# Kernel optimization log

Measured on AMD Instinct MI355X. Metric: run time of the kernel, lower is better.

Reference implementation:

```python
import jax, jax.numpy as jnp
import numpy as np
import math

HIDDEN = 768
HEADS = 12
HEAD_DIM = HIDDEN // HEADS
BLOCK = 256
TOPK = 3
BATCH = 2
SEQ = 2048


def setup_inputs() -> dict:
    key = jax.random.key(0)
    ks = jax.random.split(key, 5)
    s = 1.0 / math.sqrt(HIDDEN)
    return {
        "hidden_states": jax.random.normal(ks[0], (BATCH, SEQ, HIDDEN), jnp.float32),
        "Wq": jax.random.normal(ks[1], (HIDDEN, HIDDEN), jnp.float32) * s,
        "Wk": jax.random.normal(ks[2], (HIDDEN, HIDDEN), jnp.float32) * s,
        "Wv": jax.random.normal(ks[3], (HIDDEN, HIDDEN), jnp.float32) * s,
        "Wo": jax.random.normal(ks[4], (HIDDEN, HIDDEN), jnp.float32) * s,
    }


def _rope(x, sin, cos):
    # x: [B, H, S, D]; rotate-half RoPE
    d2 = x.shape[-1] // 2
    x1, x2 = x[..., :d2], x[..., d2:]
    return x * cos + jnp.concatenate([-x2, x1], axis=-1) * sin


def reference(hidden_states, Wq, Wk, Wv, Wo):
    B, S, Hd = hidden_states.shape
    H, D, bs, K = HEADS, HEAD_DIM, BLOCK, TOPK
    nb = S // bs  # number of key blocks
    scale = 1.0 / math.sqrt(D)

    def split_heads(x):
        return x.reshape(B, S, H, D).transpose(0, 2, 1, 3)  # [B,H,S,D]

    q = split_heads(hidden_states @ Wq.T)
    k = split_heads(hidden_states @ Wk.T)
    v = split_heads(hidden_states @ Wv.T)

    # rotary embedding (standard rotate-half RoPE, base 10000)
    inv_freq = 1.0 / (10000.0 ** (jnp.arange(0, D, 2, dtype=jnp.float32) / D))
    ang = jnp.arange(S, dtype=jnp.float32)[:, None] * inv_freq[None, :]  # [S, D/2]
    emb = jnp.concatenate([ang, ang], axis=-1)  # [S, D]
    sin, cos = jnp.sin(emb), jnp.cos(emb)
    q = _rope(q, sin, cos)
    k = _rope(k, sin, cos)

    # mean-pooled block representations of keys: [B,H,nb,D]
    block_reps = k.reshape(B, H, nb, bs, D).mean(axis=3)

    # routing scores: per-token score against each block rep
    bscores = jnp.einsum('bhsd,bhnd->bhsn', q, block_reps) * scale  # [B,H,S,nb]
    pos = jnp.arange(S)
    cur = pos // bs                       # current block of each query, [S]
    blk = jnp.arange(nb)
    future = blk[None, None, None, :] > cur[None, None, :, None]
    bscores = jnp.where(future, -jnp.inf, bscores)
    # current block is force-selected (score set to dtype max)
    is_cur = blk[None, None, None, :] == cur[None, None, :, None]
    bscores = jnp.where(is_cur, jnp.finfo(bscores.dtype).max, bscores)

    _, topk_idx = jax.lax.top_k(bscores, min(K, nb))  # [B,H,S,K]
    selected = jnp.sum(jax.nn.one_hot(topk_idx, nb, dtype=jnp.float32), axis=-2) > 0  # [B,H,S,nb]

    # per-key-position mask: key t allowed iff its block is selected for query i,
    # and within the current block only t <= i (matches original truncation).
    sel_t = selected[:, :, :, cur]                          # [B,H,Sq,Sk]
    intra_ok = (cur[None, :] != cur[:, None]) | (pos[None, :] <= pos[:, None])  # [Sq,Sk]
    mask = sel_t & intra_ok[None, None]

    scores = jnp.einsum('bhqd,bhkd->bhqk', q, k) * scale
    scores = jnp.where(mask, scores, -jnp.inf)
    probs = jax.nn.softmax(scores, axis=-1)
    out = jnp.einsum('bhqk,bhkd->bhqd', probs, v)

    out = out.transpose(0, 2, 1, 3).reshape(B, S, Hd)
    return out @ Wo.T
```

## Files before the change

kernel.cpp:

```cpp
#include <hip/hip_runtime.h>
#include <math.h>


#define HID   768
#define NH    12
#define DH    64
#define SEQN  2048
#define BATCH 2
#define NTOK  (BATCH*SEQN)
#define NB    8
#define BLKSZ 256
#define NEG_INF (-__builtin_huge_valf())
#define POS_INF (__builtin_huge_valf())
#define LO_SCALE 2048.0f
#define LO_INV   (1.0f/2048.0f)
#define EXP2C    0.18033688f

#define SPLIT_ROWS 1024
#define NBH   (BATCH*NH)

typedef unsigned short u16;
typedef _Float16 v8hf __attribute__((ext_vector_type(8)));
typedef float    v4f  __attribute__((ext_vector_type(4)));

__device__ __forceinline__ u16 f2h(float x) {
    _Float16 h = (_Float16)x;
    return __builtin_bit_cast(u16, h);
}
__device__ __forceinline__ float h2f(u16 u) {
    return (float)__builtin_bit_cast(_Float16, u);
}
__device__ __forceinline__ v8hf ldhf8(const u16* p) {
    return *reinterpret_cast<const v8hf*>(p);
}
__device__ __forceinline__ void g2lds16(const u16* g, u16* l) {
    __builtin_amdgcn_global_load_lds(
        (const __attribute__((address_space(1))) void*)g,
        (__attribute__((address_space(3))) void*)l, 16, 0, 0);
}
#define MFMA16(a, b, c) __builtin_amdgcn_mfma_f32_16x16x32_f16(a, b, c, 0, 0, 0)

__device__ const int g_uord[48] = {
    46,47,44,45,15,
    42,43,40,41,14,
    38,39,36,37,13,
    34,35,32,33,12,
    30,31,28,29,11,
    26,27,24,25,10,
    22,23,20,21, 9,
    18,19,16,17, 8,
     7, 6, 5, 4, 3, 2, 1, 0
};

__global__ __launch_bounds__(256)
void preproc_k(const float* __restrict__ X,  const float* __restrict__ Wq,
               const float* __restrict__ Wk, const float* __restrict__ Wv,
               const float* __restrict__ Wo, float2* __restrict__ tab,
               u16* __restrict__ Xh, u16* __restrict__ Xl,
               u16* __restrict__ Wq2, u16* __restrict__ Wk2,
               u16* __restrict__ Wv2, u16* __restrict__ Wo2)
{
    const int NW = HID * HID;
    const int id = blockIdx.x;
    const int tid = threadIdx.x;
    if (id < 12288) {
        const int i = id * 256 + tid;
        const float x = X[i];
        const u16 h = f2h(x);
        Xh[i] = h;
        Xl[i] = f2h((x - h2f(h)) * LO_SCALE);
    } else if (id < 21504) {
        const int j = (id - 12288) * 256 + tid;
        const int z = j / NW, i = j - z * NW;
        const float* src = (z == 0) ? Wq : (z == 1) ? Wk : (z == 2) ? Wv : Wo;
        u16* dst = (z == 0) ? Wq2 : (z == 1) ? Wk2 : (z == 2) ? Wv2 : Wo2;
        const float x = src[i];
        const u16 h = f2h(x);
        dst[i] = h;
        dst[i + NW] = f2h((x - h2f(h)) * LO_SCALE);
    } else {
        const int i = (id - 21504) * 256 + tid;
        const int s = i >> 5, f = i & 31;
        const double y  = exp((double)f * (log(10000.0) / 32.0));
        const float yf = (float)y;
        const float invf = 1.0f / yf;
        const float ang  = (float)s * invf;
        tab[i] = make_float2((float)sin((double)ang), (float)cos((double)ang));
    }
}

__device__ __forceinline__
void qkv_mainloop(const u16* __restrict__ Ah, const u16* __restrict__ Al,
                  const u16* __restrict__ Bh, const u16* __restrict__ Bl,
                  int m0, int nb0, int c_start,
                  u16* As, u16* Bs, v4f acc[2][4])
{
    const int tid = threadIdx.x;
    const int w = tid >> 6, lane = tid & 63;
    const int col = lane & 15, quad = lane >> 4;

    int a_row[4], a_gl[4];
    #pragma unroll
    for (int r = 0; r < 4; r++) {
        const int g = r * 256 + tid;
        a_row[r] = g >> 3;
        a_gl[r]  = (g & 7) ^ (a_row[r] & 7);
    }
    int b_row[2], b_gl[2];
    #pragma unroll
    for (int r = 0; r < 2; r++) {
        const int g = r * 256 + tid;
        b_row[r] = g >> 3;
        b_gl[r]  = (g & 7) ^ (b_row[r] & 7);
    }

    for (int c = c_start; c < 3; c++) {
        const u16* Ap = (c == 0) ? Al : Ah;
        const u16* Bp = (c == 1) ? Bl : Bh;
        for (int itc = 0; itc < HID / 64; itc++) {
            const int k0 = itc * 64;
            __syncthreads();
            #pragma unroll
            for (int r = 0; r < 4; r++)
                g2lds16(Ap + (size_t)(m0 + a_row[r]) * HID + k0 + a_gl[r] * 8,
                        &As[(r * 256 + w * 64) * 8]);
            #pragma unroll
            for (int r = 0; r < 2; r++)
                g2lds16(Bp + (size_t)(nb0 + b_row[r]) * HID + k0 + b_gl[r] * 8,
                        &Bs[(r * 256 + w * 64) * 8]);
            __syncthreads();
            #pragma unroll
            for (int ks = 0; ks < 2; ks++) {
                v8hf af[2], bf_[4];
                #pragma unroll
                for (int mt = 0; mt < 2; mt++) {
                    const int row = w * 32 + mt * 16 + col;
                    const int gph = (ks * 4 + quad) ^ (row & 7);
                    af[mt] = ldhf8(&As[row * 64 + gph * 8]);
                }
                #pragma unroll
                for (int nt = 0; nt < 4; nt++) {
                    const int row = nt * 16 + col;
                    const int gph = (ks * 4 + quad) ^ (row & 7);
                    bf_[nt] = ldhf8(&Bs[row * 64 + gph * 8]);
                }
                #pragma unroll
                for (int mt = 0; mt < 2; mt++)
                    #pragma unroll
                    for (int nt = 0; nt < 4; nt++)
                        acc[mt][nt] = MFMA16(af[mt], bf_[nt], acc[mt][nt]);
            }
        }
        if (c == 1) {
            #pragma unroll
            for (int mt = 0; mt < 2; mt++)
                #pragma unroll
                for (int nt = 0; nt < 4; nt++)
                    #pragma unroll
                    for (int r = 0; r < 4; r++)
                        acc[mt][nt][r] *= LO_INV;
        }
    }
    __syncthreads();
}

__global__ __launch_bounds__(256)
void qkv_fused_gemm_k(const u16* __restrict__ Xh, const u16* __restrict__ Xl,
                      const u16* __restrict__ Wq2, const u16* __restrict__ Wk2,
                      const u16* __restrict__ Wv2, const float2* __restrict__ tab,
                      float* __restrict__ q32, u16* __restrict__ kh16,
                      u16* __restrict__ vth, float* __restrict__ partial)
{
    __shared__ u16 As[128 * 64];
    __shared__ u16 Bs[64 * 64];
    __shared__ float psum[4][64];

    const int NW = HID * HID;
    const int id    = blockIdx.x;
    const int xcd   = id & 7, loc = id >> 3;
    const int mtile = xcd * 4 + (loc & 3);
    const int ntile = loc >> 2;
    const int m0  = mtile * 128;
    const int mat = ntile / 12;
    const int nb0 = (ntile - mat * 12) * 64;
    const u16* Bh = (mat == 0) ? Wq2 : (mat == 1) ? Wk2 : Wv2;

    v4f acc[2][4] = {};
    qkv_mainloop(Xh, Xl, Bh, Bh + NW, m0, nb0, (mat == 2) ? 1 : 0, As, Bs, acc);

    const int tid = threadIdx.x;
    const int w = tid >> 6, lane = tid & 63;
    const int col = lane & 15, quad = lane >> 4;
    const int b = m0 >> 11;
    const int h = nb0 >> 6;
    const size_t bh = (size_t)b * NH + h;

    if (mat == 2) {
        #pragma unroll
        for (int nt = 0; nt < 4; nt++) {
            const int d = nt * 16 + col;
            #pragma unroll
            for (int mt = 0; mt < 2; mt++) {
                const int m = m0 + w * 32 + mt * 16 + quad * 4;
                const int s = m & (SEQN - 1);
                ushort4 pk = make_ushort4(f2h(acc[mt][nt][0]), f2h(acc[mt][nt][1]),
                                          f2h(acc[mt][nt][2]), f2h(acc[mt][nt][3]));
                *(ushort4*)&vth[(bh * DH + d) * SEQN + s] = pk;
            }
        }
        return;
    }

    float vsum[4] = {0.f, 0.f, 0.f, 0.f};
    #pragma unroll
    for (int mt = 0; mt < 2; mt++) {
        #pragma unroll
        for (int nt = 0; nt < 4; nt++) {
            const int d = nt * 16 + col;
            #pragma unroll
            for (int r = 0; r < 4; r++) {
                const int m = m0 + w * 32 + mt * 16 + quad * 4 + r;
                const int s = m & (SEQN - 1);
                const float part = acc[mt][nt ^ 2][r];
                const float2 sc = tab[(s << 5) + (d & 31)];
                const float val = (d < 32) ? acc[mt][nt][r] * sc.y - part * sc.x
                                           : acc[mt][nt][r] * sc.y + part * sc.x;
                const size_t idx = (bh * SEQN + s) * DH + d;
                if (mat == 0) {
                    q32[idx] = val;
                } else {
                    kh16[idx] = f2h(val);
                    vsum[nt] += val;
                }
            }
        }
    }
    if (mat == 1) {
        #pragma unroll
        for (int nt = 0; nt < 4; nt++) {
            float v = vsum[nt];
            v += __shfl_xor(v, 16);
            v += __shfl_xor(v, 32);
            if (quad == 0) psum[w][nt * 16 + col] = v;
        }
        __syncthreads();
        if (tid < 64) {
            const float s4 = (psum[0][tid] + psum[1][tid])
                           + (psum[2][tid] + psum[3][tid]);
            const int nblk = (m0 & (SEQN - 1)) >> 8;
            const int half = (m0 >> 7) & 1;
            partial[((bh * NB + nblk) * 2 + half) * 64 + tid] = s4;
        }
    }
}

__global__ __launch_bounds__(256)
void out_gemm_mfma_k(const u16* __restrict__ Ah, const u16* __restrict__ Wo2,
                     float* __restrict__ C)
{
    __shared__ u16 As[64 * 64];
    __shared__ u16 Bs[64 * 64];

    const int NW = HID * HID;
    const int id    = blockIdx.x;
    const int xcd   = id & 7, loc = id >> 3;
    const int mtile = xcd * 8 + (loc & 7);
    const int ntile = loc >> 3;
    const int m0 = mtile * 64, n0 = ntile * 64;
    const int tid = threadIdx.x;
    const int w = tid >> 6, lane = tid & 63;
    const int col = lane & 15, quad = lane >> 4;

    const int r0 = tid >> 3,         gl0 = (tid & 7) ^ (r0 & 7);
    const int r1 = (256 + tid) >> 3, gl1 = ((256 + tid) & 7) ^ (r1 & 7);

    v4f acc[4] = {};
    #pragma unroll
    for (int c = 0; c < 2; c++) {
        const u16* Bp = (c == 0) ? (Wo2 + NW) : Wo2;
        for (int itc = 0; itc < HID / 64; itc++) {
            const int k0 = itc * 64;
            __syncthreads();
            g2lds16(Ah + (size_t)(m0 + r0) * HID + k0 + gl0 * 8, &As[(w * 64) * 8]);
            g2lds16(Ah + (size_t)(m0 + r1) * HID + k0 + gl1 * 8, &As[(256 + w * 64) * 8]);
            g2lds16(Bp + (size_t)(n0 + r0) * HID + k0 + gl0 * 8, &Bs[(w * 64) * 8]);
            g2lds16(Bp + (size_t)(n0 + r1) * HID + k0 + gl1 * 8, &Bs[(256 + w * 64) * 8]);
            __syncthreads();
            #pragma unroll
            for (int ks = 0; ks < 2; ks++) {
                const int arow = w * 16 + col;
                v8hf a = ldhf8(&As[arow * 64 + (((ks * 4 + quad) ^ (arow & 7))) * 8]);
                #pragma unroll
                for (int nt = 0; nt < 4; nt++) {
                    const int row = nt * 16 + col;
                    v8hf bb = ldhf8(&Bs[row * 64 + (((ks * 4 + quad) ^ (row & 7))) * 8]);
                    acc[nt] = MFMA16(a, bb, acc[nt]);
                }
            }
        }
        if (c == 0) {
            #pragma unroll
            for (int nt = 0; nt < 4; nt++)
                #pragma unroll
                for (int r = 0; r < 4; r++)
                    acc[nt][r] *= LO_INV;
        }
    }

    #pragma unroll
    for (int nt = 0; nt < 4; nt++)
        #pragma unroll
        for (int r = 0; r < 4; r++) {
            const int m = m0 + w * 16 + quad * 4 + r;
            C[(size_t)m * HID + n0 + nt * 16 + col] = acc[nt][r];
        }
}

__global__ __launch_bounds__(64)
void reps_reduce_k(const float* __restrict__ partial, float* __restrict__ reps)
{
    const int bhn = blockIdx.x;
    const int d = threadIdx.x;
    const float* p = &partial[(size_t)bhn * 128 + d];
    double s = (double)p[0] + (double)p[64];
    reps[(size_t)bhn * 64 + d] = (float)(s * (1.0 / 256.0));
}

__global__ __launch_bounds__(128)
void select_topk_k(const float* __restrict__ qg, const float* __restrict__ reps,
                   unsigned* __restrict__ selm)
{
    __shared__ float rs[NB][DH];
    const int bh = blockIdx.y;
    const int tid = threadIdx.x;
    for (int idx = tid; idx < NB * DH; idx += 128)
        rs[idx >> 6][idx & 63] = reps[(size_t)bh * NB * DH + idx];
    __syncthreads();

    const int qq = blockIdx.x * 128 + tid;
    const float* qv = &qg[((size_t)bh * SEQN + qq) * DH];
    float qr[DH];
    #pragma unroll
    for (int c = 0; c < 16; c++) {
        float4 t = *(const float4*)&qv[c * 4];
        qr[c*4+0]=t.x; qr[c*4+1]=t.y; qr[c*4+2]=t.z; qr[c*4+3]=t.w;
    }
    const int cur = qq >> 8;
    double sc[NB];
    #pragma unroll
    for (int n = 0; n < NB; n++) {
        double ssum = 0.0;
        for (int d = 0; d < DH; d++) ssum += (double)qr[d] * (double)rs[n][d];
        sc[n] = ssum * 0.125;
    }
    for (int n = cur + 1; n < NB; n++) sc[n] = -1e300;
    sc[cur] = 1e300;
    unsigned mask = 0;
    for (int p = 0; p < 3; p++) {
        int bi = -1; double bv = 0.0;
        for (int n = 0; n < NB; n++) {
            if ((mask >> n) & 1) continue;
            if (bi < 0 || sc[n] > bv) { bi = n; bv = sc[n]; }
        }
        mask |= 1u << bi;
    }
    selm[(size_t)bh * SEQN + qq] = mask;
}

__global__ __launch_bounds__(256, 4)
void moba_attn_k(const float* __restrict__ q32, const u16* __restrict__ kh16,
                 const u16* __restrict__ vth, const unsigned* __restrict__ selm,
                 u16* __restrict__ aoh, float* __restrict__ po,
                 float* __restrict__ ml)
{
    __shared__ u16 kbuf[2][64 * 64];
    __shared__ u16 vbuf[2][64 * 64];
    __shared__ u16 plds[4][16][64];
    unsigned* s_uni = (unsigned*)&vbuf[1][0];

    const int id  = blockIdx.x;
    const int xcd = id & 7, loc = id >> 3;
    const int bh  = xcd * 3 + loc / 48;
    const int u   = g_uord[loc % 48];
    int qb, split, stride;
    if (u < 16) { qb = u;                 split = 0;          stride = 1; }
    else        { qb = 16 + ((u - 16) >> 1); split = (u - 16) & 1; stride = 2; }
    const int q0  = qb * 64;
    const int cur = q0 >> 8;
    const int tid = threadIdx.x;
    const int wave = tid >> 6, lane = tid & 63;
    const int col = lane & 15, quad = lane >> 4;
    const int qw0 = q0 + wave * 16;
    const int qpos = qw0 + col;
    const size_t bhS = (size_t)bh * SEQN;
    const size_t bhV = (size_t)bh * DH;

    if (tid == 0) *s_uni = 0;
    __syncthreads();
    const unsigned mymask = selm[bhS + qw0 + col];
    unsigned uw = mymask;
    #pragma unroll
    for (int off = 1; off < 16; off <<= 1) uw |= __shfl_xor(uw, off);
    if (lane == 0) atomicOr(s_uni, uw);
    const unsigned wmask = __builtin_amdgcn_readfirstlane(uw);

    v8hf qh[2], ql[2];
    #pragma unroll
    for (int ks = 0; ks < 2; ks++) {
        const float* qp = &q32[(bhS + qw0 + col) * DH + ks * 32 + quad * 8];
        float4 f0 = *(const float4*)qp;
        float4 f1 = *(const float4*)(qp + 4);
        float qf[8] = {f0.x, f0.y, f0.z, f0.w, f1.x, f1.y, f1.z, f1.w};
        union { u16 u[8]; v8hf h; } uh, ul;
        #pragma unroll
        for (int j = 0; j < 8; j++) {
            u16 hb = f2h(qf[j]);
            uh.u[j] = hb;
            ul.u[j] = f2h((qf[j] - h2f(hb)) * LO_SCALE);
        }
        qh[ks] = uh.h; ql[ks] = ul.h;
    }
    __syncthreads();
    const unsigned uni = __builtin_amdgcn_readfirstlane(*s_uni);

    int n_nxt = __builtin_ctz(uni), c_nxt = 0;
    bool has_nxt = true;
    auto c2max = [&](int n) { return (n == cur) ? ((q0 + 63 - n * BLKSZ) >> 6) : 3; };
    auto advance1 = [&]() {
        if (c_nxt < c2max(n_nxt)) { c_nxt++; return; }
        for (int nn = n_nxt + 1; nn < NB; nn++)
            if ((uni >> nn) & 1) { n_nxt = nn; c_nxt = 0; return; }
        has_nxt = false;
    };
    for (int i = 0; i < split; i++) if (has_nxt) advance1();
    int n_cur = n_nxt, c_cur = c_nxt;
    const bool cur_valid = has_nxt;

    const size_t srow0 = (size_t)bh * SPLIT_ROWS + (q0 - SPLIT_ROWS);

    if (!cur_valid) {
        if (stride == 2) {
            if (quad == 0) {
                const size_t r = srow0 + wave * 16 + col;
                ml[(r * 2 + split) * 2 + 0] = NEG_INF;
                ml[(r * 2 + split) * 2 + 1] = 0.f;
            }
            #pragma unroll
            for (int nt = 0; nt < 4; nt++)
                #pragma unroll
                for (int r = 0; r < 4; r++) {
                    const size_t rq = srow0 + wave * 16 + quad * 4 + r;
                    po[(rq * 2 + split) * 64 + nt * 16 + col] = 0.f;
                }
        }
        return;
    }
    for (int i = 0; i < stride; i++) if (has_nxt) advance1();

    const int sg_row0 = tid >> 3;
    const int sg_gl0  = (tid & 7) ^ (sg_row0 & 7);
    const int sg_row1 = (256 + tid) >> 3;
    const int sg_gl1  = ((256 + tid) & 7) ^ (sg_row1 & 7);
    auto stage = [&](int n, int c2, int buf) {
        const int kb = n * BLKSZ + c2 * 64;
        u16* kd = (u16*)kbuf[buf];
        u16* vd = (u16*)vbuf[buf];
        const size_t ks0 = (bhS + kb + sg_row0) * DH + sg_gl0 * 8;
        const size_t ks1 = (bhS + kb + sg_row1) * DH + sg_gl1 * 8;
        const size_t vs0 = (bhV + sg_row0) * SEQN + kb + sg_gl0 * 8;
        const size_t vs1 = (bhV + sg_row1) * SEQN + kb + sg_gl1 * 8;
        g2lds16(kh16 + ks0, kd + (wave * 64) * 8);
        g2lds16(kh16 + ks1, kd + (256 + wave * 64) * 8);
        g2lds16(vth + vs0, vd + (wave * 64) * 8);
        g2lds16(vth + vs1, vd + (256 + wave * 64) * 8);
    };

    const v4f zero4 = {0.f, 0.f, 0.f, 0.f};
    v4f oacc[4] = {zero4, zero4, zero4, zero4};
    float m_i = NEG_INF, l_i = 0.f;
    const int psw = (col & 7) << 1;

    stage(n_cur, c_cur, 0);
    int t = 0;
    while (true) {
        __syncthreads();
        if (has_nxt) stage(n_nxt, c_nxt, (t + 1) & 1);

        const int n  = n_cur;
        const int kb = n * BLKSZ + c_cur * 64;
        const bool iscur = (n == cur);
        const float selinf = ((mymask >> n) & 1) ? 0.f : POS_INF;
        const bool need_mask = iscur && (kb + 63 > qw0);
        const u16* kd = (const u16*)kbuf[t & 1];
        const u16* vd = (const u16*)vbuf[t & 1];

        if ((wmask >> n) & 1) {
            v4f sf[4];
            __builtin_amdgcn_s_setprio(1);
            #pragma unroll
            for (int mt = 0; mt < 4; mt++) {
                const int row = mt * 16 + col;
                const int r7 = row & 7;
                v8hf kh0 = ldhf8(&kd[(row * 8 + (quad ^ r7)) * 8]);
                v8hf kh1 = ldhf8(&kd[(row * 8 + ((4 + quad) ^ r7)) * 8]);
                v4f c = zero4;
                c = MFMA16(kh0, ql[0], c);
                c = MFMA16(kh1, ql[1], c);
                #pragma unroll
                for (int r = 0; r < 4; r++) c[r] *= LO_INV;
                c = MFMA16(kh0, qh[0], c);
                c = MFMA16(kh1, qh[1], c);
                sf[mt] = c;
            }
            __builtin_amdgcn_s_setprio(0);

            if (need_mask) {
                #pragma unroll
                for (int mt = 0; mt < 4; mt++)
                    #pragma unroll
                    for (int r = 0; r < 4; r++) {
                        const int kidx = kb + mt * 16 + quad * 4 + r;
                        sf[mt][r] = (kidx <= qpos) ? sf[mt][r] : NEG_INF;
                    }
            }

            float rm = NEG_INF;
            #pragma unroll
            for (int mt = 0; mt < 4; mt++)
                #pragma unroll
                for (int r = 0; r < 4; r++) rm = fmaxf(rm, sf[mt][r]);
            rm = fmaxf(rm, __shfl_xor(rm, 16));
            rm = fmaxf(rm, __shfl_xor(rm, 32));
            rm = rm - selinf;
            const float mnew  = fmaxf(m_i, rm);
            const float alpha = (m_i == NEG_INF) ? 0.f : exp2f((m_i - mnew) * EXP2C);
            const float biasC = ((mnew == NEG_INF) ? 0.f : mnew * EXP2C) + selinf;

            float lsum = 0.f;
            #pragma unroll
            for (int mt = 0; mt < 4; mt++) {
                ushort4 hv;
                #pragma unroll
                for (int r = 0; r < 4; r++) {
                    float p = exp2f(fmaf(sf[mt][r], EXP2C, -biasC));
                    lsum += p;
                    u16 hu = f2h(p);
                    if (r == 0) hv.x = hu;
                    else if (r == 1) hv.y = hu;
                    else if (r == 2) hv.z = hu;
                    else hv.w = hu;
                }
                *(ushort4*)&plds[wave][col][((mt * 4 + quad) ^ psw) * 4] = hv;
            }
            lsum += __shfl_xor(lsum, 16);
            lsum += __shfl_xor(lsum, 32);
            l_i = l_i * alpha + lsum;
            m_i = mnew;

            float ar[4];
            #pragma unroll
            for (int r = 0; r < 4; r++) ar[r] = __shfl(alpha, quad * 4 + r, 16);
            #pragma unroll
            for (int nt = 0; nt < 4; nt++)
                #pragma unroll
                for (int r = 0; r < 4; r++) oacc[nt][r] *= ar[r];

            __threadfence_block();

            __builtin_amdgcn_s_setprio(1);
            #pragma unroll
            for (int ks2 = 0; ks2 < 2; ks2++) {
                v8hf ph = ldhf8(&plds[wave][col][((ks2 * 8 + quad * 2) ^ psw) * 4]);
                #pragma unroll
                for (int nt = 0; nt < 4; nt++) {
                    const int row = nt * 16 + col;
                    const int g = (ks2 * 4 + quad) ^ (row & 7);
                    v8hf vh = ldhf8(&vd[(row * 8 + g) * 8]);
                    oacc[nt] = MFMA16(ph, vh, oacc[nt]);
                }
            }
            __builtin_amdgcn_s_setprio(0);
        }

        if (!has_nxt) break;
        n_cur = n_nxt; c_cur = c_nxt;
        for (int i = 0; i < stride; i++) if (has_nxt) advance1();
        t++;
    }

    if (stride == 2) {
        if (quad == 0) {
            const size_t r = srow0 + wave * 16 + col;
            ml[(r * 2 + split) * 2 + 0] = m_i;
            ml[(r * 2 + split) * 2 + 1] = l_i;
        }
        #pragma unroll
        for (int nt = 0; nt < 4; nt++)
            #pragma unroll
            for (int r = 0; r < 4; r++) {
                const size_t rq = srow0 + wave * 16 + quad * 4 + r;
                po[(rq * 2 + split) * 64 + nt * 16 + col] = oacc[nt][r];
            }
        return;
    }

    const int b = bh / NH, h = bh % NH;
    const float invl = 1.f / l_i;
    float ir[4];
    #pragma unroll
    for (int r = 0; r < 4; r++) ir[r] = __shfl(invl, quad * 4 + r, 16);
    #pragma unroll
    for (int nt = 0; nt < 4; nt++)
        #pragma unroll
        for (int r = 0; r < 4; r++) {
            const int qi = qw0 + quad * 4 + r;
            const size_t idx = ((size_t)b * SEQN + qi) * HID + h * DH + nt * 16 + col;
            aoh[idx] = f2h(oacc[nt][r] * ir[r]);
        }
}

__global__ __launch_bounds__(256)
void attn_combine_k(const float* __restrict__ po, const float* __restrict__ ml,
                    u16* __restrict__ aoh)
{
    const int g = blockIdx.x * 256 + threadIdx.x;
    const int d = g & 63;
    const size_t row = (size_t)(g >> 6);
    const int bh = (int)(row >> 10);
    const int qlocal = (int)(row & 1023);
    const float m0 = ml[(row * 2 + 0) * 2 + 0], l0 = ml[(row * 2 + 0) * 2 + 1];
    const float m1 = ml[(row * 2 + 1) * 2 + 0], l1 = ml[(row * 2 + 1) * 2 + 1];
    const float m  = fmaxf(m0, m1);
    const float a0 = (m0 == NEG_INF) ? 0.f : exp2f((m0 - m) * EXP2C);
    const float a1 = (m1 == NEG_INF) ? 0.f : exp2f((m1 - m) * EXP2C);
    const float o  = po[(row * 2 + 0) * 64 + d] * a0
                   + po[(row * 2 + 1) * 64 + d] * a1;
    const float inv = 1.f / (l0 * a0 + l1 * a1);
    const int b = bh / NH, h = bh % NH;
    const int q = SPLIT_ROWS + qlocal;
    aoh[((size_t)b * SEQN + q) * HID + h * DH + d] = f2h(o * inv);
}

extern "C" void kernel_launch(void* const* d_in, const int* in_sizes, int n_in,
                              void* d_out, int out_size, void* d_ws, size_t ws_size,
                              hipStream_t stream)
{
    const float* X  = (const float*)d_in[0];
    const float* Wq = (const float*)d_in[1];
    const float* Wk = (const float*)d_in[2];
    const float* Wv = (const float*)d_in[3];
    const float* Wo = (const float*)d_in[4];
    float* out = (float*)d_out;

    char* p = (char*)d_ws;
    float* q32 = (float*)p;                p += (size_t)NTOK*HID*4;
    u16* kh16 = (u16*)p;                   p += (size_t)NTOK*HID*2;
    u16* vth  = (u16*)p;                   p += (size_t)NTOK*HID*2;
    u16* Xh   = (u16*)p;                   p += (size_t)NTOK*HID*2;
    u16* Xl   = (u16*)p;                   p += (size_t)NTOK*HID*2;
    u16* Wq2  = (u16*)p;                   p += (size_t)HID*HID*2*2;
    u16* Wk2  = (u16*)p;                   p += (size_t)HID*HID*2*2;
    u16* Wv2  = (u16*)p;                   p += (size_t)HID*HID*2*2;
    u16* Wo2  = (u16*)p;                   p += (size_t)HID*HID*2*2;
    float* partial = (float*)p;            p += (size_t)BATCH*NH*NB*2*64*4;
    float* reps    = (float*)p;            p += (size_t)BATCH*NH*NB*DH*4;
    unsigned* selm = (unsigned*)p;         p += (size_t)BATCH*NH*SEQN*4;
    float2* tab    = (float2*)p;           p += (size_t)SEQN*32*8;
    u16* aoh = Xh;

    float* po = (float*)Xl;
    float* ml = po + (size_t)NBH * SPLIT_ROWS * 2 * 64;

    preproc_k<<<dim3(21760), 256, 0, stream>>>(X, Wq, Wk, Wv, Wo, tab,
                                               Xh, Xl, Wq2, Wk2, Wv2, Wo2);

    qkv_fused_gemm_k<<<dim3(1152), 256, 0, stream>>>(
        Xh, Xl, Wq2, Wk2, Wv2, tab, q32, kh16, vth, partial);

    reps_reduce_k<<<dim3(BATCH*NH*NB), 64, 0, stream>>>(partial, reps);
    select_topk_k<<<dim3(SEQN/128, BATCH*NH), 128, 0, stream>>>(q32, reps, selm);

    moba_attn_k<<<dim3(1152), 256, 0, stream>>>(
        q32, kh16, vth, selm, aoh, po, ml);

    attn_combine_k<<<dim3(6144), 256, 0, stream>>>(po, ml, aoh);

    out_gemm_mfma_k<<<dim3(768), 256, 0, stream>>>(aoh, Wo2, out);
}
```

Measured before the change: 220.2 us.

## Fuse split-fp16 correction passes into single K loop sharing staged operand tiles

The QKV and output GEMMs previously ran up to three separate K passes (lo*hi, hi*lo, hi*hi), reloading the X and weight tiles each pass. Now a single K loop stages the hi and lo halves of both operands together in doubled LDS buffers and issues all the MFMAs per tile into two accumulators, combining them at the end. This cuts global/LDS tile reloads and barrier rounds, at the cost of more LDS per block and extra accumulator registers; launch bounds now request a minimum of 3 blocks per CU to keep occupancy.

```diff
diff --git a/kernel.cpp b/kernel.cpp
--- a/kernel.cpp
+++ b/kernel.cpp
@@ -92,12 +92,13 @@
 __device__ __forceinline__
 void qkv_mainloop(const u16* __restrict__ Ah, const u16* __restrict__ Al,
                   const u16* __restrict__ Bh, const u16* __restrict__ Bl,
-                  int m0, int nb0, int c_start,
-                  u16* As, u16* Bs, v4f acc[2][4])
+                  int m0, int nb0, bool hasC0,
+                  u16* As, u16* Bs, v4f acc01[2][4], v4f acc2[2][4])
 {
     const int tid = threadIdx.x;
     const int w = tid >> 6, lane = tid & 63;
     const int col = lane & 15, quad = lane >> 4;
+    const int AOFF = 128 * 64, BOFF = 64 * 64;
 
     int a_row[4], a_gl[4];
     #pragma unroll
@@ -114,66 +115,68 @@
         b_gl[r]  = (g & 7) ^ (b_row[r] & 7);
     }
 
-    for (int c = c_start; c < 3; c++) {
-        const u16* Ap = (c == 0) ? Al : Ah;
-        const u16* Bp = (c == 1) ? Bl : Bh;
-        for (int itc = 0; itc < HID / 64; itc++) {
-            const int k0 = itc * 64;
-            __syncthreads();
+    for (int itc = 0; itc < HID / 64; itc++) {
+        const int k0 = itc * 64;
+        __syncthreads();
+        #pragma unroll
+        for (int r = 0; r < 4; r++)
+            g2lds16(Ah + (size_t)(m0 + a_row[r]) * HID + k0 + a_gl[r] * 8,
+                    &As[(r * 256 + w * 64) * 8]);
+        if (hasC0) {
             #pragma unroll
             for (int r = 0; r < 4; r++)
-                g2lds16(Ap + (size_t)(m0 + a_row[r]) * HID + k0 + a_gl[r] * 8,
-                        &As[(r * 256 + w * 64) * 8]);
-            #pragma unroll
-            for (int r = 0; r < 2; r++)
-                g2lds16(Bp + (size_t)(nb0 + b_row[r]) * HID + k0 + b_gl[r] * 8,
-                        &Bs[(r * 256 + w * 64) * 8]);
-            __syncthreads();
-            #pragma unroll
-            for (int ks = 0; ks < 2; ks++) {
-                v8hf af[2], bf_[4];
-                #pragma unroll
-                for (int mt = 0; mt < 2; mt++) {
-                    const int row = w * 32 + mt * 16 + col;
-                    const int gph = (ks * 4 + quad) ^ (row & 7);
-                    af[mt] = ldhf8(&As[row * 64 + gph * 8]);
+                g2lds16(Al + (size_t)(m0 + a_row[r]) * HID + k0 + a_gl[r] * 8,
+                        &As[AOFF + (r * 256 + w * 64) * 8]);
+        }
+        #pragma unroll
+        for (int r = 0; r < 2; r++) {
+            g2lds16(Bh + (size_t)(nb0 + b_row[r]) * HID + k0 + b_gl[r] * 8,
+                    &Bs[(r * 256 + w * 64) * 8]);
+            g2lds16(Bl + (size_t)(nb0 + b_row[r]) * HID + k0 + b_gl[r] * 8,
+                    &Bs[BOFF + (r * 256 + w * 64) * 8]);
+        }
+        __syncthreads();
+        #pragma unroll
+        for (int ks = 0; ks < 2; ks++) {
+            v8hf afh[2], afl[2], bfh[4], bfl[4];
+            #pragma unroll
+            for (int mt = 0; mt < 2; mt++) {
+                const int row = w * 32 + mt * 16 + col;
+                const int gph = (ks * 4 + quad) ^ (row & 7);
+                afh[mt] = ldhf8(&As[row * 64 + gph * 8]);
+                if (hasC0) afl[mt] = ldhf8(&As[AOFF + row * 64 + gph * 8]);
+            }
+            #pragma unroll
+            for (int nt = 0; nt < 4; nt++) {
+                const int row = nt * 16 + col;
+                const int gph = (ks * 4 + quad) ^ (row & 7);
+                bfh[nt] = ldhf8(&Bs[row * 64 + gph * 8]);
+                bfl[nt] = ldhf8(&Bs[BOFF + row * 64 + gph * 8]);
+            }
+            #pragma unroll
+            for (int mt = 0; mt < 2; mt++)
+                #pragma unroll
+                for (int nt = 0; nt < 4; nt++) {
+                    if (hasC0)
+                        acc01[mt][nt] = MFMA16(afl[mt], bfh[nt], acc01[mt][nt]);
+                    acc01[mt][nt] = MFMA16(afh[mt], bfl[nt], acc01[mt][nt]);
+                    acc2[mt][nt]  = MFMA16(afh[mt], bfh[nt], acc2[mt][nt]);
                 }
-                #pragma unroll
-                for (int nt = 0; nt < 4; nt++) {
-                    const int row = nt * 16 + col;
-                    const int gph = (ks * 4 + quad) ^ (row & 7);
-                    bf_[nt] = ldhf8(&Bs[row * 64 + gph * 8]);
-                }
-                #pragma unroll
-                for (int mt = 0; mt < 2; mt++)
-                    #pragma unroll
-                    for (int nt = 0; nt < 4; nt++)
-                        acc[mt][nt] = MFMA16(af[mt], bf_[nt], acc[mt][nt]);
-            }
-        }
-        if (c == 1) {
-            #pragma unroll
-            for (int mt = 0; mt < 2; mt++)
-                #pragma unroll
-                for (int nt = 0; nt < 4; nt++)
-                    #pragma unroll
-                    for (int r = 0; r < 4; r++)
-                        acc[mt][nt][r] *= LO_INV;
         }
     }
     __syncthreads();
 }
 
-__global__ __launch_bounds__(256)
+__global__ __launch_bounds__(256, 3)
 void qkv_fused_gemm_k(const u16* __restrict__ Xh, const u16* __restrict__ Xl,
                       const u16* __restrict__ Wq2, const u16* __restrict__ Wk2,
                       const u16* __restrict__ Wv2, const float2* __restrict__ tab,
                       float* __restrict__ q32, u16* __restrict__ kh16,
                       u16* __restrict__ vth, float* __restrict__ partial)
 {
-    __shared__ u16 As[128 * 64];
-    __shared__ u16 Bs[64 * 64];
-    __shared__ float psum[4][64];
+    __shared__ u16 As[2 * 128 * 64];
+    __shared__ u16 Bs[2 * 64 * 64];
+    float (*psum)[64] = (float(*)[64])As;
 
     const int NW = HID * HID;
     const int id    = blockIdx.x;
@@ -185,8 +188,17 @@
     const int nb0 = (ntile - mat * 12) * 64;
     const u16* Bh = (mat == 0) ? Wq2 : (mat == 1) ? Wk2 : Wv2;
 
-    v4f acc[2][4] = {};
-    qkv_mainloop(Xh, Xl, Bh, Bh + NW, m0, nb0, (mat == 2) ? 1 : 0, As, Bs, acc);
+    v4f acc01[2][4] = {}, acc2[2][4] = {};
+    qkv_mainloop(Xh, Xl, Bh, Bh + NW, m0, nb0, mat != 2, As, Bs, acc01, acc2);
+
+    v4f acc[2][4];
+    #pragma unroll
+    for (int mt = 0; mt < 2; mt++)
+        #pragma unroll
+        for (int nt = 0; nt < 4; nt++)
+            #pragma unroll
+            for (int r = 0; r < 4; r++)
+                acc[mt][nt][r] = acc01[mt][nt][r] * LO_INV + acc2[mt][nt][r];
 
     const int tid = threadIdx.x;
     const int w = tid >> 6, lane = tid & 63;
@@ -254,12 +266,13 @@
     }
 }
 
-__global__ __launch_bounds__(256)
+__global__ __launch_bounds__(256, 3)
 void out_gemm_mfma_k(const u16* __restrict__ Ah, const u16* __restrict__ Wo2,
                      float* __restrict__ C)
 {
     __shared__ u16 As[64 * 64];
-    __shared__ u16 Bs[64 * 64];
+    __shared__ u16 Bs[2 * 64 * 64];
+    const int BOFF = 64 * 64;
 
     const int NW = HID * HID;
     const int id    = blockIdx.x;
@@ -274,36 +287,31 @@
     const int r0 = tid >> 3,         gl0 = (tid & 7) ^ (r0 & 7);
     const int r1 = (256 + tid) >> 3, gl1 = ((256 + tid) & 7) ^ (r1 & 7);
 
-    v4f acc[4] = {};
-    #pragma unroll
-    for (int c = 0; c < 2; c++) {
-        const u16* Bp = (c == 0) ? (Wo2 + NW) : Wo2;
-        for (int itc = 0; itc < HID / 64; itc++) {
-            const int k0 = itc * 64;
-            __syncthreads();
-            g2lds16(Ah + (size_t)(m0 + r0) * HID + k0 + gl0 * 8, &As[(w * 64) * 8]);
-            g2lds16(Ah + (size_t)(m0 + r1) * HID + k0 + gl1 * 8, &As[(256 + w * 64) * 8]);
-            g2lds16(Bp + (size_t)(n0 + r0) * HID + k0 + gl0 * 8, &Bs[(w * 64) * 8]);
-            g2lds16(Bp + (size_t)(n0 + r1) * HID + k0 + gl1 * 8, &Bs[(256 + w * 64) * 8]);
-            __syncthreads();
-            #pragma unroll
-            for (int ks = 0; ks < 2; ks++) {
-                const int arow = w * 16 + col;
-                v8hf a = ldhf8(&As[arow * 64 + (((ks * 4 + quad) ^ (arow & 7))) * 8]);
-                #pragma unroll
-                for (int nt = 0; nt < 4; nt++) {
-                    const int row = nt * 16 + col;
-                    v8hf bb = ldhf8(&Bs[row * 64 + (((ks * 4 + quad) ^ (row & 7))) * 8]);
-                    acc[nt] = MFMA16(a, bb, acc[nt]);
-                }
-            }
-        }
-        if (c == 0) {
-            #pragma unroll
-            for (int nt = 0; nt < 4; nt++)
-                #pragma unroll
-                for (int r = 0; r < 4; r++)
-                    acc[nt][r] *= LO_INV;
+    const u16* Bhp = Wo2;
+    const u16* Blp = Wo2 + NW;
+
+    v4f accL[4] = {}, accH[4] = {};
+    for (int itc = 0; itc < HID / 64; itc++) {
+        const int k0 = itc * 64;
+        __syncthreads();
+        g2lds16(Ah  + (size_t)(m0 + r0) * HID + k0 + gl0 * 8, &As[(w * 64) * 8]);
+        g2lds16(Ah  + (size_t)(m0 + r1) * HID + k0 + gl1 * 8, &As[(256 + w * 64) * 8]);
+        g2lds16(Bhp + (size_t)(n0 + r0) * HID + k0 + gl0 * 8, &Bs[(w * 64) * 8]);
+        g2lds16(Bhp + (size_t)(n0 + r1) * HID + k0 + gl1 * 8, &Bs[(256 + w * 64) * 8]);
+        g2lds16(Blp + (size_t)(n0 + r0) * HID + k0 + gl0 * 8, &Bs[BOFF + (w * 64) * 8]);
+        g2lds16(Blp + (size_t)(n0 + r1) * HID + k0 + gl1 * 8, &Bs[BOFF + (256 + w * 64) * 8]);
+        __syncthreads();
+        #pragma unroll
+        for (int ks = 0; ks < 2; ks++) {
+            const int arow = w * 16 + col;
+            v8hf a = ldhf8(&As[arow * 64 + (((ks * 4 + quad) ^ (arow & 7))) * 8]);
+            #pragma unroll
+            for (int nt = 0; nt < 4; nt++) {
+                const int row = nt * 16 + col;
+                const int g = (ks * 4 + quad) ^ (row & 7);
+                accH[nt] = MFMA16(a, ldhf8(&Bs[row * 64 + g * 8]), accH[nt]);
+                accL[nt] = MFMA16(a, ldhf8(&Bs[BOFF + row * 64 + g * 8]), accL[nt]);
+            }
         }
     }
 
@@ -312,7 +320,8 @@
         #pragma unroll
         for (int r = 0; r < 4; r++) {
             const int m = m0 + w * 16 + quad * 4 + r;
-            C[(size_t)m * HID + n0 + nt * 16 + col] = acc[nt][r];
+            C[(size_t)m * HID + n0 + nt * 16 + col] =
+                accL[nt][r] * LO_INV + accH[nt][r];
         }
 }
 
```

Result: faster. 214.3 us (-2.7%).
